# Performance work log

Measured on AMD Instinct MI355X. Metric: run time of the kernel, lower is better.

Reference implementation:

```python
import jax, jax.numpy as jnp
import numpy as np

RNN = 50
FEAT = 128
NCLS = 8
ALPHA = 0.3  # keras LeakyReLU default


def setup_inputs() -> dict:
    key = jax.random.key(0)
    ks = jax.random.split(key, 6)
    B, T = 256, 2048
    x = jax.random.normal(ks[0], (B, T, FEAT), dtype=jnp.float32)
    # GRU params (Keras layout: kernel [F,3H], recurrent [H,3H], bias [2,3H] for reset_after=True)
    W = jax.random.normal(ks[1], (FEAT, 3 * RNN), dtype=jnp.float32) / np.sqrt(FEAT)
    U = jax.random.normal(ks[2], (RNN, 3 * RNN), dtype=jnp.float32) / np.sqrt(RNN)
    b = jax.random.normal(ks[3], (2, 3 * RNN), dtype=jnp.float32) * 0.01
    W2 = jax.random.normal(ks[4], (RNN, NCLS), dtype=jnp.float32) / np.sqrt(RNN)
    b2 = jnp.zeros((NCLS,), dtype=jnp.float32)
    return {"inputs": x, "W": W, "U": U, "b": b, "W2": W2, "b2": b2}


def _gru_last_state(x, W, U, b):
    # x: [B,T,F] -> precompute input projections [T,B,3H]
    B = x.shape[0]
    xw = jnp.einsum("btf,fh->tbh", x, W) + b[0]
    h0 = jnp.zeros((B, RNN), dtype=x.dtype)

    def step(h, xt):
        inner = h @ U + b[1]                       # [B,3H]
        z = jax.nn.sigmoid(xt[:, :RNN] + inner[:, :RNN])
        r = jax.nn.sigmoid(xt[:, RNN:2 * RNN] + inner[:, RNN:2 * RNN])
        hh = jnp.tanh(xt[:, 2 * RNN:] + r * inner[:, 2 * RNN:])
        h_new = z * h + (1.0 - z) * hh
        return h_new, None

    h_last, _ = jax.lax.scan(step, h0, xw)
    return h_last  # [B,H]


def reference(inputs, W, U, b, W2, b2):
    h = _gru_last_state(inputs, W, U, b)
    h = jnp.where(h >= 0, h, ALPHA * h)            # LeakyReLU(0.3)
    logits = h @ W2 + b2
    return jax.nn.softmax(logits, axis=-1)
```

## Files before the change

### kernel.cpp

```cpp
#include <hip/hip_runtime.h>

typedef __attribute__((ext_vector_type(4))) float f32x4;
typedef _Float16 f16;
typedef __attribute__((ext_vector_type(2))) _Float16 f16x2;
typedef __attribute__((ext_vector_type(8))) _Float16 f16x8;

#define T_LEN 2048
#define B_SZ 256
#define FEATN 128
#define H 50
#define H3 150
#define XW_STRIDE 160

__device__ __forceinline__ float rcpf(float x) { return __builtin_amdgcn_rcpf(x); }

__device__ __forceinline__ float dot2f(f16x2 a, f16x2 b, float c) {
#if __has_builtin(__builtin_amdgcn_fdot2)
  return __builtin_amdgcn_fdot2(a, b, c, false);
#else
  return fmaf((float)a[1], (float)b[1], fmaf((float)a[0], (float)b[0], c));
#endif
}

__global__ __launch_bounds__(256) void xw_gemm(const float* __restrict__ x,
                                               const float* __restrict__ W,
                                               f16* __restrict__ xw) {
  __shared__ f16 Wt[160 * 136];
  const int tid = threadIdx.x;
  for (int idx = tid; idx < FEATN * H3; idx += 256) {
    int f = idx / H3;
    int n = idx - f * H3;
    Wt[n * 136 + f] = (f16)W[idx];
  }
  for (int idx = tid; idx < 10 * FEATN; idx += 256) {
    int n = H3 + (idx >> 7);
    int f = idx & 127;
    Wt[n * 136 + f] = (f16)0.f;
  }
  __syncthreads();

  const int wid = tid >> 6;
  const int lane = tid & 63;
  const int l15 = lane & 15;
  const int g = lane >> 4;
  const long row0 = (long)blockIdx.x * 128 + wid * 32;

  f16x8 a[2][4];
#pragma unroll
  for (int sub = 0; sub < 2; ++sub) {
    const float* xp = x + (row0 + sub * 16 + l15) * FEATN + g * 8;
#pragma unroll
    for (int kk = 0; kk < 4; ++kk) {
      f32x4 p0 = *(const f32x4*)(xp + kk * 32);
      f32x4 p1 = *(const f32x4*)(xp + kk * 32 + 4);
      f16x8 v;
      v[0] = (f16)p0[0]; v[1] = (f16)p0[1]; v[2] = (f16)p0[2]; v[3] = (f16)p0[3];
      v[4] = (f16)p1[0]; v[5] = (f16)p1[1]; v[6] = (f16)p1[2]; v[7] = (f16)p1[3];
      a[sub][kk] = v;
    }
  }

  for (int nt = 0; nt < 10; ++nt) {
    const f16* bp = &Wt[(nt * 16 + l15) * 136 + g * 8];
    f16x8 bf0 = *(const f16x8*)(bp);
    f16x8 bf1 = *(const f16x8*)(bp + 32);
    f16x8 bf2 = *(const f16x8*)(bp + 64);
    f16x8 bf3 = *(const f16x8*)(bp + 96);
    f32x4 acc0 = {0.f, 0.f, 0.f, 0.f};
    f32x4 acc1 = {0.f, 0.f, 0.f, 0.f};
    acc0 = __builtin_amdgcn_mfma_f32_16x16x32_f16(a[0][0], bf0, acc0, 0, 0, 0);
    acc0 = __builtin_amdgcn_mfma_f32_16x16x32_f16(a[0][1], bf1, acc0, 0, 0, 0);
    acc0 = __builtin_amdgcn_mfma_f32_16x16x32_f16(a[0][2], bf2, acc0, 0, 0, 0);
    acc0 = __builtin_amdgcn_mfma_f32_16x16x32_f16(a[0][3], bf3, acc0, 0, 0, 0);
    acc1 = __builtin_amdgcn_mfma_f32_16x16x32_f16(a[1][0], bf0, acc1, 0, 0, 0);
    acc1 = __builtin_amdgcn_mfma_f32_16x16x32_f16(a[1][1], bf1, acc1, 0, 0, 0);
    acc1 = __builtin_amdgcn_mfma_f32_16x16x32_f16(a[1][2], bf2, acc1, 0, 0, 0);
    acc1 = __builtin_amdgcn_mfma_f32_16x16x32_f16(a[1][3], bf3, acc1, 0, 0, 0);
    int col = nt * 16 + l15;
    if (col < H3) {
#pragma unroll
      for (int r = 0; r < 4; ++r) {
        long rowA = row0 + g * 4 + r;
        xw[rowA * XW_STRIDE + col] = (f16)acc0[r];
        xw[(rowA + 16) * XW_STRIDE + col] = (f16)acc1[r];
      }
    }
  }
}

__global__ __launch_bounds__(64, 1) void gru_head64(const f16* __restrict__ xw,
                                                    const float* __restrict__ U,
                                                    const float* __restrict__ bias,
                                                    const float* __restrict__ W2,
                                                    const float* __restrict__ b2,
                                                    float* __restrict__ out) {
  __shared__ __align__(16) f16 h_lds16[64];
  __shared__ float fin[52];
  __shared__ float red[8];
  const int l = threadIdx.x;
  const int b = blockIdx.x;
  const int lc = l < H ? l : H - 1;
  const bool act = l < H;
  const long base = (long)b * T_LEN * XW_STRIDE;

  f16x2 uz2[25], ur2[25], uh2[25];
#pragma unroll
  for (int c = 0; c < 25; ++c) {
    uz2[c][0] = (f16)U[(2 * c) * H3 + lc];
    uz2[c][1] = (f16)U[(2 * c + 1) * H3 + lc];
    ur2[c][0] = (f16)U[(2 * c) * H3 + H + lc];
    ur2[c][1] = (f16)U[(2 * c + 1) * H3 + H + lc];
    uh2[c][0] = (f16)U[(2 * c) * H3 + 2 * H + lc];
    uh2[c][1] = (f16)U[(2 * c + 1) * H3 + 2 * H + lc];
  }
  const float bz = bias[lc] + bias[H3 + lc];
  const float br = bias[H + lc] + bias[H3 + H + lc];
  const float b0h = bias[2 * H + lc];
  const float b1h = bias[H3 + 2 * H + lc];

  float hreg = 0.f;
  h_lds16[l] = (f16)0.f;

  f16 pz[8], pr[8], ph[8];
#pragma unroll
  for (int p = 0; p < 8; ++p) {
    long o = base + (long)p * XW_STRIDE;
    pz[p] = xw[o + lc];
    pr[p] = xw[o + H + lc];
    ph[p] = xw[o + 2 * H + lc];
  }

  const f16x8* hp8 = (const f16x8*)h_lds16;

  for (int t0 = 0; t0 < T_LEN; t0 += 8) {
#define STEP(P)                                                               \
    {                                                                         \
      f16x8 w0 = hp8[0], w1 = hp8[1], w2 = hp8[2];                            \
      f16x8 w3 = hp8[3], w4 = hp8[4], w5 = hp8[5];                            \
      f16x2 w6 = *(const f16x2*)(h_lds16 + 48);                               \
      float xzf = (float)pz[P];                                               \
      float xrf = (float)pr[P];                                               \
      float xhf = (float)ph[P];                                               \
      {                                                                       \
        int tn = (t0 + (P) + 8) & (T_LEN - 1);                                \
        long o = base + (long)tn * XW_STRIDE;                                 \
        pz[P] = xw[o + lc];                                                   \
        pr[P] = xw[o + H + lc];                                               \
        ph[P] = xw[o + 2 * H + lc];                                           \
      }                                                                       \
      f16x2 hv[25];                                                           \
      hv[0] = __builtin_shufflevector(w0, w0, 0, 1);                          \
      hv[1] = __builtin_shufflevector(w0, w0, 2, 3);                          \
      hv[2] = __builtin_shufflevector(w0, w0, 4, 5);                          \
      hv[3] = __builtin_shufflevector(w0, w0, 6, 7);                          \
      hv[4] = __builtin_shufflevector(w1, w1, 0, 1);                          \
      hv[5] = __builtin_shufflevector(w1, w1, 2, 3);                          \
      hv[6] = __builtin_shufflevector(w1, w1, 4, 5);                          \
      hv[7] = __builtin_shufflevector(w1, w1, 6, 7);                          \
      hv[8] = __builtin_shufflevector(w2, w2, 0, 1);                          \
      hv[9] = __builtin_shufflevector(w2, w2, 2, 3);                          \
      hv[10] = __builtin_shufflevector(w2, w2, 4, 5);                         \
      hv[11] = __builtin_shufflevector(w2, w2, 6, 7);                         \
      hv[12] = __builtin_shufflevector(w3, w3, 0, 1);                         \
      hv[13] = __builtin_shufflevector(w3, w3, 2, 3);                         \
      hv[14] = __builtin_shufflevector(w3, w3, 4, 5);                         \
      hv[15] = __builtin_shufflevector(w3, w3, 6, 7);                         \
      hv[16] = __builtin_shufflevector(w4, w4, 0, 1);                         \
      hv[17] = __builtin_shufflevector(w4, w4, 2, 3);                         \
      hv[18] = __builtin_shufflevector(w4, w4, 4, 5);                         \
      hv[19] = __builtin_shufflevector(w4, w4, 6, 7);                         \
      hv[20] = __builtin_shufflevector(w5, w5, 0, 1);                         \
      hv[21] = __builtin_shufflevector(w5, w5, 2, 3);                         \
      hv[22] = __builtin_shufflevector(w5, w5, 4, 5);                         \
      hv[23] = __builtin_shufflevector(w5, w5, 6, 7);                         \
      hv[24] = w6;                                                            \
      float sr0 = br, sr1 = 0.f;                                              \
      _Pragma("unroll")                                                       \
      for (int p = 0; p < 25; ++p) {                                          \
        if (p & 1) sr1 = dot2f(hv[p], ur2[p], sr1);                           \
        else sr0 = dot2f(hv[p], ur2[p], sr0);                                 \
      }                                                                       \
      float ar = (sr0 + sr1) + xrf;                                           \
      float rr = rcpf(1.f + __expf(-ar));                                     \
      float sh0 = b1h, sh1 = 0.f;                                             \
      _Pragma("unroll")                                                       \
      for (int p = 0; p < 25; ++p) {                                          \
        if (p & 1) sh1 = dot2f(hv[p], uh2[p], sh1);                           \
        else sh0 = dot2f(hv[p], uh2[p], sh0);                                 \
      }                                                                       \
      float ah = fmaf(rr, sh0 + sh1, xhf + b0h);                              \
      float eh = __expf(-2.f * ah);                                           \
      float sz0 = bz, sz1 = 0.f;                                              \
      _Pragma("unroll")                                                       \
      for (int p = 0; p < 25; ++p) {                                          \
        if (p & 1) sz1 = dot2f(hv[p], uz2[p], sz1);                           \
        else sz0 = dot2f(hv[p], uz2[p], sz0);                                 \
      }                                                                       \
      float az = (sz0 + sz1) + xzf;                                           \
      float zz = rcpf(1.f + __expf(-az));                                     \
      float th = fmaf(2.f, rcpf(1.f + eh), -1.f);                             \
      hreg = fmaf(zz, hreg - th, th);                                         \
      h_lds16[l] = (f16)hreg;                                                 \
    }
    STEP(0) STEP(1) STEP(2) STEP(3) STEP(4) STEP(5) STEP(6) STEP(7)
#undef STEP
  }

  if (act) {
    fin[l] = hreg >= 0.f ? hreg : 0.3f * hreg;
  }
  if (l < 8) {
    float acc = b2[l];
#pragma unroll
    for (int j = 0; j < H; ++j) acc = fmaf(fin[j], W2[j * 8 + l], acc);
    red[l] = acc;
  }
  if (l < 8) {
    float m = red[0];
#pragma unroll
    for (int i = 1; i < 8; ++i) m = fmaxf(m, red[i]);
    float s = 0.f;
#pragma unroll
    for (int i = 0; i < 8; ++i) s += __expf(red[i] - m);
    out[b * 8 + l] = __expf(red[l] - m) / s;
  }
}

extern "C" void kernel_launch(void* const* d_in, const int* in_sizes, int n_in,
                              void* d_out, int out_size, void* d_ws, size_t ws_size,
                              hipStream_t stream) {
  const float* x = (const float*)d_in[0];
  const float* W = (const float*)d_in[1];
  const float* U = (const float*)d_in[2];
  const float* bias = (const float*)d_in[3];
  const float* W2 = (const float*)d_in[4];
  const float* b2 = (const float*)d_in[5];
  float* out = (float*)d_out;
  f16* xw = (f16*)d_ws;

  xw_gemm<<<4096, 256, 0, stream>>>(x, W, xw);
  gru_head64<<<256, 64, 0, stream>>>(xw, U, bias, W2, b2, out);
}
```

Baseline: 724.8 us.

## Interleave gate dot products, shorten prefetch window, pin weights in VGPRs

The three gate dot-product loops are merged into one interleaved loop so the z, r and h accumulations issue together and the exponentials for r and z can overlap. The xw prefetch depth drops from 8 to 4 steps and uses a pointer that advances each iteration; a peeled final iteration removes the wraparound mask. Empty asm statements pin the U weights and biases in registers so the compiler cannot rematerialize or spill them. This trades instruction-level parallelism against prefetch latency hiding and adds register pressure.

New measurement: 613.1 us. -15.4%, faster.

```diff
diff --git a/kernel.cpp b/kernel.cpp
--- a/kernel.cpp
+++ b/kernel.cpp
@@ -113,41 +113,58 @@
     uh2[c][0] = (f16)U[(2 * c) * H3 + 2 * H + lc];
     uh2[c][1] = (f16)U[(2 * c + 1) * H3 + 2 * H + lc];
   }
-  const float bz = bias[lc] + bias[H3 + lc];
-  const float br = bias[H + lc] + bias[H3 + H + lc];
-  const float b0h = bias[2 * H + lc];
-  const float b1h = bias[H3 + 2 * H + lc];
+  float bz = bias[lc] + bias[H3 + lc];
+  float br = bias[H + lc] + bias[H3 + H + lc];
+  float b0h = bias[2 * H + lc];
+  float b1h = bias[H3 + 2 * H + lc];
 
   float hreg = 0.f;
   h_lds16[l] = (f16)0.f;
 
-  f16 pz[8], pr[8], ph[8];
-#pragma unroll
-  for (int p = 0; p < 8; ++p) {
-    long o = base + (long)p * XW_STRIDE;
-    pz[p] = xw[o + lc];
-    pr[p] = xw[o + H + lc];
-    ph[p] = xw[o + 2 * H + lc];
+  const f16* q = xw + base + lc;
+
+  f16 pz[4], pr[4], ph[4];
+#pragma unroll
+  for (int p = 0; p < 4; ++p) {
+    pz[p] = q[p * XW_STRIDE];
+    pr[p] = q[p * XW_STRIDE + H];
+    ph[p] = q[p * XW_STRIDE + 2 * H];
   }
 
   const f16x8* hp8 = (const f16x8*)h_lds16;
 
-  for (int t0 = 0; t0 < T_LEN; t0 += 8) {
-#define STEP(P)                                                               \
+#define PINS()                                                                \
+  asm volatile("" : "+v"(uz2[0]), "+v"(uz2[1]), "+v"(uz2[2]), "+v"(uz2[3]),  \
+                    "+v"(uz2[4]), "+v"(uz2[5]), "+v"(uz2[6]), "+v"(uz2[7]),  \
+                    "+v"(uz2[8]), "+v"(uz2[9]), "+v"(uz2[10]), "+v"(uz2[11]),\
+                    "+v"(uz2[12]), "+v"(uz2[13]), "+v"(uz2[14]),             \
+                    "+v"(uz2[15]), "+v"(uz2[16]), "+v"(uz2[17]),             \
+                    "+v"(uz2[18]), "+v"(uz2[19]), "+v"(uz2[20]),             \
+                    "+v"(uz2[21]), "+v"(uz2[22]), "+v"(uz2[23]),             \
+                    "+v"(uz2[24]));                                          \
+  asm volatile("" : "+v"(ur2[0]), "+v"(ur2[1]), "+v"(ur2[2]), "+v"(ur2[3]),  \
+                    "+v"(ur2[4]), "+v"(ur2[5]), "+v"(ur2[6]), "+v"(ur2[7]),  \
+                    "+v"(ur2[8]), "+v"(ur2[9]), "+v"(ur2[10]), "+v"(ur2[11]),\
+                    "+v"(ur2[12]), "+v"(ur2[13]), "+v"(ur2[14]),             \
+                    "+v"(ur2[15]), "+v"(ur2[16]), "+v"(ur2[17]),             \
+                    "+v"(ur2[18]), "+v"(ur2[19]), "+v"(ur2[20]),             \
+                    "+v"(ur2[21]), "+v"(ur2[22]), "+v"(ur2[23]),             \
+                    "+v"(ur2[24]));                                          \
+  asm volatile("" : "+v"(uh2[0]), "+v"(uh2[1]), "+v"(uh2[2]), "+v"(uh2[3]),  \
+                    "+v"(uh2[4]), "+v"(uh2[5]), "+v"(uh2[6]), "+v"(uh2[7]),  \
+                    "+v"(uh2[8]), "+v"(uh2[9]), "+v"(uh2[10]), "+v"(uh2[11]),\
+                    "+v"(uh2[12]), "+v"(uh2[13]), "+v"(uh2[14]),             \
+                    "+v"(uh2[15]), "+v"(uh2[16]), "+v"(uh2[17]),             \
+                    "+v"(uh2[18]), "+v"(uh2[19]), "+v"(uh2[20]),             \
+                    "+v"(uh2[21]), "+v"(uh2[22]), "+v"(uh2[23]),             \
+                    "+v"(uh2[24]));                                          \
+  asm volatile("" : "+v"(bz), "+v"(br), "+v"(b0h), "+v"(b1h));
+
+#define STEP(P, PF)                                                           \
     {                                                                         \
       f16x8 w0 = hp8[0], w1 = hp8[1], w2 = hp8[2];                            \
       f16x8 w3 = hp8[3], w4 = hp8[4], w5 = hp8[5];                            \
       f16x2 w6 = *(const f16x2*)(h_lds16 + 48);                               \
-      float xzf = (float)pz[P];                                               \
-      float xrf = (float)pr[P];                                               \
-      float xhf = (float)ph[P];                                               \
-      {                                                                       \
-        int tn = (t0 + (P) + 8) & (T_LEN - 1);                                \
-        long o = base + (long)tn * XW_STRIDE;                                 \
-        pz[P] = xw[o + lc];                                                   \
-        pr[P] = xw[o + H + lc];                                               \
-        ph[P] = xw[o + 2 * H + lc];                                           \
-      }                                                                       \
       f16x2 hv[25];                                                           \
       hv[0] = __builtin_shufflevector(w0, w0, 0, 1);                          \
       hv[1] = __builtin_shufflevector(w0, w0, 2, 3);                          \
@@ -174,37 +191,50 @@
       hv[22] = __builtin_shufflevector(w5, w5, 4, 5);                         \
       hv[23] = __builtin_shufflevector(w5, w5, 6, 7);                         \
       hv[24] = w6;                                                            \
-      float sr0 = br, sr1 = 0.f;                                              \
+      float sz0 = bz, sr0 = br, sh0 = b1h;                                    \
+      float sz1 = 0.f, sr1 = 0.f, sh1 = 0.f;                                  \
       _Pragma("unroll")                                                       \
       for (int p = 0; p < 25; ++p) {                                          \
-        if (p & 1) sr1 = dot2f(hv[p], ur2[p], sr1);                           \
-        else sr0 = dot2f(hv[p], ur2[p], sr0);                                 \
+        if (p & 1) {                                                          \
+          sz1 = dot2f(hv[p], uz2[p], sz1);                                    \
+          sr1 = dot2f(hv[p], ur2[p], sr1);                                    \
+          sh1 = dot2f(hv[p], uh2[p], sh1);                                    \
+        } else {                                                              \
+          sz0 = dot2f(hv[p], uz2[p], sz0);                                    \
+          sr0 = dot2f(hv[p], ur2[p], sr0);                                    \
+          sh0 = dot2f(hv[p], uh2[p], sh0);                                    \
+        }                                                                     \
+      }                                                                       \
+      float xzf = (float)pz[P];                                               \
+      float xrf = (float)pr[P];                                               \
+      float xhf = (float)ph[P];                                               \
+      if (PF) {                                                               \
+        pz[P] = q[(P + 4) * XW_STRIDE];                                       \
+        pr[P] = q[(P + 4) * XW_STRIDE + H];                                   \
+        ph[P] = q[(P + 4) * XW_STRIDE + 2 * H];                               \
       }                                                                       \
       float ar = (sr0 + sr1) + xrf;                                           \
-      float rr = rcpf(1.f + __expf(-ar));                                     \
-      float sh0 = b1h, sh1 = 0.f;                                             \
-      _Pragma("unroll")                                                       \
-      for (int p = 0; p < 25; ++p) {                                          \
-        if (p & 1) sh1 = dot2f(hv[p], uh2[p], sh1);                           \
-        else sh0 = dot2f(hv[p], uh2[p], sh0);                                 \
-      }                                                                       \
+      float er = __expf(-ar);                                                 \
+      float az = (sz0 + sz1) + xzf;                                           \
+      float ez = __expf(-az);                                                 \
+      float rr = rcpf(1.f + er);                                              \
+      float zz = rcpf(1.f + ez);                                              \
       float ah = fmaf(rr, sh0 + sh1, xhf + b0h);                              \
       float eh = __expf(-2.f * ah);                                           \
-      float sz0 = bz, sz1 = 0.f;                                              \
-      _Pragma("unroll")                                                       \
-      for (int p = 0; p < 25; ++p) {                                          \
-        if (p & 1) sz1 = dot2f(hv[p], uz2[p], sz1);                           \
-        else sz0 = dot2f(hv[p], uz2[p], sz0);                                 \
-      }                                                                       \
-      float az = (sz0 + sz1) + xzf;                                           \
-      float zz = rcpf(1.f + __expf(-az));                                     \
       float th = fmaf(2.f, rcpf(1.f + eh), -1.f);                             \
       hreg = fmaf(zz, hreg - th, th);                                         \
       h_lds16[l] = (f16)hreg;                                                 \
     }
-    STEP(0) STEP(1) STEP(2) STEP(3) STEP(4) STEP(5) STEP(6) STEP(7)
+
+  for (int t0 = 0; t0 < T_LEN - 4; t0 += 4) {
+    PINS()
+    STEP(0, 1) STEP(1, 1) STEP(2, 1) STEP(3, 1)
+    q += 4 * XW_STRIDE;
+  }
+  PINS()
+  STEP(0, 0) STEP(1, 0) STEP(2, 0) STEP(3, 0)
 #undef STEP
-  }
+#undef PINS
 
   if (act) {
     fin[l] = hreg >= 0.f ? hreg : 0.3f * hreg;
```
